# Kernel tuning notes

Hardware: AMD Instinct MI355X
Metric: run time of the kernel (lower is better)

## Reference

```python
import jax, jax.numpy as jnp
import numpy as np


def _fft(x_real, x_imag):
    # Recursive radix-2 Cooley-Tukey, decimation in time.
    # N is static (256), so the recursion fully unrolls at trace time.
    N = x_real.shape[-1]
    if N == 1:
        return x_real, x_imag
    even_real, even_imag = _fft(x_real[..., ::2], x_imag[..., ::2])
    odd_real, odd_imag = _fft(x_real[..., 1::2], x_imag[..., 1::2])
    k = jnp.arange(N // 2, dtype=jnp.float32).reshape(1, -1)
    angle = -2.0 * jnp.pi * k / float(N)
    cos = jnp.cos(angle)
    sin = jnp.sin(angle)
    t_real = cos * odd_real - sin * odd_imag
    t_imag = cos * odd_imag + sin * odd_real
    real = jnp.concatenate([even_real + t_real, even_real - t_real], axis=-1)
    imag = jnp.concatenate([even_imag + t_imag, even_imag - t_imag], axis=-1)
    return real, imag


def setup_inputs() -> dict:
    key = jax.random.key(0)
    x = jax.random.normal(key, (131072, 2, 256), dtype=jnp.float32)
    return {"x": x}


def reference(x):
    # x: [B, 2, 256] (real/imag channels)
    real, imag = _fft(x[:, 0, :], x[:, 1, :])
    return jnp.stack([real, imag], axis=1)
```

## Files before the change

kernel.cpp:

```cpp
#include <hip/hip_runtime.h>
#include <math.h>


#define NB 16
#define TS 272

__device__ __forceinline__ void wave_fence() {
    __builtin_amdgcn_wave_barrier();
}

__device__ __forceinline__ void fft16(float re[16], float im[16]) {
    {
        float tr, ti;
#define SWP(a, b) tr = re[a]; re[a] = re[b]; re[b] = tr; ti = im[a]; im[a] = im[b]; im[b] = ti;
        SWP(1, 8) SWP(2, 4) SWP(3, 12) SWP(5, 10) SWP(7, 14) SWP(11, 13)
#undef SWP
    }
    const float C[8] = { 1.0f,  0.92387953251f,  0.70710678119f,  0.38268343236f,
                         0.0f, -0.38268343236f, -0.70710678119f, -0.92387953251f };
    const float S16[8] = { 0.0f, -0.38268343236f, -0.70710678119f, -0.92387953251f,
                          -1.0f, -0.92387953251f, -0.70710678119f, -0.38268343236f };
#pragma unroll
    for (int s = 1; s <= 4; ++s) {
        const int len = 1 << s;
        const int half = len >> 1;
        const int step = 16 >> s;
#pragma unroll
        for (int i = 0; i < 16; i += len) {
#pragma unroll
            for (int j = 0; j < half; ++j) {
                const float wr = C[j * step];
                const float wi = S16[j * step];
                const int p = i + j;
                const int q = i + j + half;
                const float vr = re[q] * wr - im[q] * wi;
                const float vi = re[q] * wi + im[q] * wr;
                const float ur = re[p], ui = im[p];
                re[p] = ur + vr; im[p] = ui + vi;
                re[q] = ur - vr; im[q] = ui - vi;
            }
        }
    }
}

__global__ __launch_bounds__(256, 4) void fft256_kernel(const float* __restrict__ x,
                                                        float* __restrict__ out) {
    __shared__ float tile[NB * TS];

    const int tid = threadIdx.x;
    const int sub = tid >> 4;
    const int t   = tid & 15;
    const long b  = (long)blockIdx.x * NB + sub;

    const float* xr = x + b * 512;
    const float* xi = xr + 256;

    float re[16], im[16];

#pragma unroll
    for (int i = 0; i < 16; ++i) re[i] = xr[t + 16 * i];
#pragma unroll
    for (int i = 0; i < 16; ++i) im[i] = xi[t + 16 * i];

    fft16(re, im);

    float* L = tile + sub * TS;

#pragma unroll
    for (int k = 0; k < 16; ++k) {
        float sv, cv;
        __sincosf(-6.283185307179586f * (float)(t * k) * (1.0f / 256.0f), &sv, &cv);
        const float tr = re[k] * cv - im[k] * sv;
        const float ti = re[k] * sv + im[k] * cv;
        L[17 * t + k] = ti;
        re[k] = tr;
    }
    wave_fence();

#pragma unroll
    for (int n = 0; n < 16; ++n) im[n] = L[17 * n + t];
    wave_fence();

#pragma unroll
    for (int k = 0; k < 16; ++k) L[17 * t + k] = re[k];
    wave_fence();
#pragma unroll
    for (int n = 0; n < 16; ++n) re[n] = L[17 * n + t];

    fft16(re, im);

    float* outr = out + b * 512;
    float* outi = outr + 256;
#pragma unroll
    for (int k = 0; k < 16; ++k) __builtin_nontemporal_store(re[k], outr + t + 16 * k);
#pragma unroll
    for (int k = 0; k < 16; ++k) __builtin_nontemporal_store(im[k], outi + t + 16 * k);
}

extern "C" void kernel_launch(void* const* d_in, const int* in_sizes, int n_in,
                              void* d_out, int out_size, void* d_ws, size_t ws_size,
                              hipStream_t stream) {
    (void)d_ws; (void)ws_size; (void)n_in; (void)out_size;
    const float* x = (const float*)d_in[0];
    float* out = (float*)d_out;
    const int batches = in_sizes[0] / 512;
    const int grid = batches / NB;
    fft256_kernel<<<grid, 256, 0, stream>>>(x, out);
}
```

Before: 96.04 us.

## Double-buffer async global-to-LDS loads across multiple tiles per block

Each block now processes four 16-batch tiles. Inputs are prefetched with global_load_lds into a double-buffered LDS stage, and manual vmcnt waits overlap the next tile's loads with the current tile's FFT and stores. The LDS stage also serves as the transpose scratch. This is meant to hide global load latency and raise achieved bandwidth, at the cost of large LDS use per block, lower occupancy and fragile hand-counted waitcnt values.

Result: slower. 100.8 us (+4.9%).

```diff
diff --git a/kernel.cpp b/kernel.cpp
--- a/kernel.cpp
+++ b/kernel.cpp
@@ -2,11 +2,16 @@
 #include <math.h>
 
 
-#define NB 16
-#define TS 272
+#define T_TILES 4
 
 __device__ __forceinline__ void wave_fence() {
     __builtin_amdgcn_wave_barrier();
+}
+
+__device__ __forceinline__ void gload16(const float* g, float* l) {
+    __builtin_amdgcn_global_load_lds(
+        (const __attribute__((address_space(1))) void*)g,
+        (__attribute__((address_space(3))) void*)l, 16, 0, 0);
 }
 
 __device__ __forceinline__ void fft16(float re[16], float im[16]) {
@@ -43,58 +48,84 @@
     }
 }
 
-__global__ __launch_bounds__(256, 4) void fft256_kernel(const float* __restrict__ x,
-                                                        float* __restrict__ out) {
-    __shared__ float tile[NB * TS];
+__global__ __launch_bounds__(256) void fft256_kernel(const float* __restrict__ x,
+                                                     float* __restrict__ out) {
+    __shared__ __align__(16) float stage[2 * 4 * 2048];
 
-    const int tid = threadIdx.x;
-    const int sub = tid >> 4;
-    const int t   = tid & 15;
-    const long b  = (long)blockIdx.x * NB + sub;
+    const int tid  = threadIdx.x;
+    const int wave = tid >> 6;
+    const int lane = tid & 63;
+    const int sub  = tid >> 4;
+    const int t16  = tid & 15;
+    const int siw  = sub & 3;
 
-    const float* xr = x + b * 512;
-    const float* xi = xr + 256;
+    const long block_base = (long)blockIdx.x * (T_TILES * 16);
 
-    float re[16], im[16];
+    float* wbuf[2] = { stage + wave * 2048, stage + 8192 + wave * 2048 };
 
 #pragma unroll
-    for (int i = 0; i < 16; ++i) re[i] = xr[t + 16 * i];
+    for (int pt = 0; pt < 2; ++pt) {
+        const float* src = x + (block_base + pt * 16 + wave * 4) * 512 + lane * 4;
+        float* dst = wbuf[pt];
 #pragma unroll
-    for (int i = 0; i < 16; ++i) im[i] = xi[t + 16 * i];
-
-    fft16(re, im);
-
-    float* L = tile + sub * TS;
+        for (int j = 0; j < 8; ++j) gload16(src + j * 256, dst + j * 256);
+    }
 
 #pragma unroll
-    for (int k = 0; k < 16; ++k) {
-        float sv, cv;
-        __sincosf(-6.283185307179586f * (float)(t * k) * (1.0f / 256.0f), &sv, &cv);
-        const float tr = re[k] * cv - im[k] * sv;
-        const float ti = re[k] * sv + im[k] * cv;
-        L[17 * t + k] = ti;
-        re[k] = tr;
-    }
-    wave_fence();
+    for (int t = 0; t < T_TILES; ++t) {
+        if (t == 0)               asm volatile("s_waitcnt vmcnt(8)" ::: "memory");
+        else if (t < T_TILES - 1) asm volatile("s_waitcnt vmcnt(40)" ::: "memory");
+        else                      asm volatile("s_waitcnt vmcnt(32)" ::: "memory");
+        __builtin_amdgcn_sched_barrier(0);
+
+        float* Ls = wbuf[t & 1] + siw * 512;
+        const long bb = block_base + t * 16 + sub;
+
+        float re[16], im[16];
+#pragma unroll
+        for (int i = 0; i < 16; ++i) re[i] = Ls[t16 + 16 * i];
+#pragma unroll
+        for (int i = 0; i < 16; ++i) im[i] = Ls[256 + t16 + 16 * i];
+
+        fft16(re, im);
 
 #pragma unroll
-    for (int n = 0; n < 16; ++n) im[n] = L[17 * n + t];
-    wave_fence();
+        for (int k = 0; k < 16; ++k) {
+            float sv, cv;
+            __sincosf(-6.283185307179586f * (float)(t16 * k) * (1.0f / 256.0f), &sv, &cv);
+            const float tr = re[k] * cv - im[k] * sv;
+            const float ti = re[k] * sv + im[k] * cv;
+            Ls[17 * t16 + k] = ti;
+            re[k] = tr;
+        }
+        wave_fence();
+#pragma unroll
+        for (int n = 0; n < 16; ++n) im[n] = Ls[17 * n + t16];
+        wave_fence();
+#pragma unroll
+        for (int k = 0; k < 16; ++k) Ls[17 * t16 + k] = re[k];
+        wave_fence();
+#pragma unroll
+        for (int n = 0; n < 16; ++n) re[n] = Ls[17 * n + t16];
 
+        fft16(re, im);
+
+        float* outr = out + bb * 512;
+        float* outi = outr + 256;
 #pragma unroll
-    for (int k = 0; k < 16; ++k) L[17 * t + k] = re[k];
-    wave_fence();
+        for (int k = 0; k < 16; ++k) __builtin_nontemporal_store(re[k], outr + t16 + 16 * k);
 #pragma unroll
-    for (int n = 0; n < 16; ++n) re[n] = L[17 * n + t];
+        for (int k = 0; k < 16; ++k) __builtin_nontemporal_store(im[k], outi + t16 + 16 * k);
 
-    fft16(re, im);
-
-    float* outr = out + b * 512;
-    float* outi = outr + 256;
+        if (t + 2 < T_TILES) {
+            asm volatile("" ::: "memory");
+            __builtin_amdgcn_sched_barrier(0);
+            const float* src = x + (block_base + (t + 2) * 16 + wave * 4) * 512 + lane * 4;
+            float* dst = wbuf[t & 1];
 #pragma unroll
-    for (int k = 0; k < 16; ++k) __builtin_nontemporal_store(re[k], outr + t + 16 * k);
-#pragma unroll
-    for (int k = 0; k < 16; ++k) __builtin_nontemporal_store(im[k], outi + t + 16 * k);
+            for (int j = 0; j < 8; ++j) gload16(src + j * 256, dst + j * 256);
+        }
+    }
 }
 
 extern "C" void kernel_launch(void* const* d_in, const int* in_sizes, int n_in,
@@ -104,6 +135,6 @@
     const float* x = (const float*)d_in[0];
     float* out = (float*)d_out;
     const int batches = in_sizes[0] / 512;
-    const int grid = batches / NB;
+    const int grid = batches / (T_TILES * 16);
     fft256_kernel<<<grid, 256, 0, stream>>>(x, out);
 }
```
